# Performance work log

Hardware: AMD Instinct MI355X
Metric: run time of the kernel (lower is better)

## Reference

```python
import jax, jax.numpy as jnp
import numpy as np

N, E, IN, HID, OUT = 40000, 640000, 128, 512, 256


def setup_inputs() -> dict:
    key = jax.random.key(0)
    ks = jax.random.split(key, 8)
    x = jax.random.normal(ks[0], (N, IN), dtype=jnp.float32)
    edge_index = jax.random.randint(ks[1], (2, E), 0, N, dtype=jnp.int64)
    # SAGEConv params: lin_l (applied to aggregated neighbors, with bias),
    # lin_r (applied to root nodes, no bias) -- PyG defaults.
    def lin(k, fin, fout):
        return jax.random.normal(k, (fin, fout), dtype=jnp.float32) / np.sqrt(fin)
    return {
        "x": x,
        "edge_index": edge_index,
        "W1l": lin(ks[2], IN, HID),
        "b1": jnp.zeros((HID,), jnp.float32),
        "W1r": lin(ks[3], IN, HID),
        "W2l": lin(ks[4], HID, OUT),
        "b2": jnp.zeros((OUT,), jnp.float32),
        "W2r": lin(ks[5], HID, OUT),
    }


def _sage_conv(x, src, dst, Wl, b, Wr):
    n = x.shape[0]
    # gather messages from source nodes, mean-aggregate at destination
    msg = x[src]                                            # [E, F]
    agg = jax.ops.segment_sum(msg, dst, num_segments=n)     # [N, F]
    cnt = jax.ops.segment_sum(jnp.ones((src.shape[0],), x.dtype), dst,
                              num_segments=n)               # [N]
    agg = agg / jnp.maximum(cnt, 1.0)[:, None]
    # out = lin_l(mean_neighbors) + lin_r(x)
    return agg @ Wl + b + x @ Wr


def reference(x, edge_index, W1l, b1, W1r, W2l, b2, W2r):
    src, dst = edge_index[0], edge_index[1]
    h = jax.nn.relu(_sage_conv(x, src, dst, W1l, b1, W1r))
    return _sage_conv(h, src, dst, W2l, b2, W2r)
```

## Files before the change

### kernel.cpp

```cpp
#include <hip/hip_runtime.h>


#define N_NODES 40000
#define N_EDGES 640000
#define F_IN 128
#define F_HID 512
#define F_OUT 256
#define NB_SCAN 157

typedef unsigned short ushort_t;
typedef __attribute__((ext_vector_type(8))) short bf16x8;
typedef __attribute__((ext_vector_type(4))) float floatx4;

__device__ __forceinline__ ushort_t f2bf(float f) {
  union { float f; unsigned int u; } x; x.f = f;
  unsigned int r = (x.u + 0x7FFFu + ((x.u >> 16) & 1u)) >> 16;
  return (ushort_t)r;
}
__device__ __forceinline__ float bf2f(ushort_t u) {
  union { unsigned int u; float f; } x; x.u = ((unsigned int)u) << 16;
  return x.f;
}

__global__ void scanA_kernel(const int* __restrict__ deg, int* __restrict__ bsum) {
  __shared__ int sdata[256];
  int i = blockIdx.x * 256 + threadIdx.x;
  sdata[threadIdx.x] = (i < N_NODES) ? deg[i] : 0;
  __syncthreads();
  #pragma unroll
  for (int off = 128; off > 0; off >>= 1) {
    if (threadIdx.x < off) sdata[threadIdx.x] += sdata[threadIdx.x + off];
    __syncthreads();
  }
  if (threadIdx.x == 0) bsum[blockIdx.x] = sdata[0];
}

__global__ void scanB_kernel(const int* __restrict__ bsum, int* __restrict__ boff) {
  __shared__ int buf[2][256];
  int tid = threadIdx.x;
  int v = (tid < NB_SCAN) ? bsum[tid] : 0;
  buf[0][tid] = v;
  __syncthreads();
  int cur = 0;
  #pragma unroll
  for (int off = 1; off < 256; off <<= 1) {
    int val = buf[cur][tid];
    if (tid >= off) val += buf[cur][tid - off];
    buf[cur ^ 1][tid] = val;
    __syncthreads();
    cur ^= 1;
  }
  if (tid < NB_SCAN) boff[tid] = buf[cur][tid] - v;
}

__global__ void scanC_kernel(const int* __restrict__ deg, const int* __restrict__ boff,
                             int* __restrict__ rowptr, int* __restrict__ cursor) {
  __shared__ int buf[2][256];
  int tid = threadIdx.x;
  int i = blockIdx.x * 256 + tid;
  int v = (i < N_NODES) ? deg[i] : 0;
  buf[0][tid] = v;
  __syncthreads();
  int cur = 0;
  #pragma unroll
  for (int off = 1; off < 256; off <<= 1) {
    int val = buf[cur][tid];
    if (tid >= off) val += buf[cur][tid - off];
    buf[cur ^ 1][tid] = val;
    __syncthreads();
    cur ^= 1;
  }
  if (i < N_NODES) {
    int ex = boff[blockIdx.x] + buf[cur][tid] - v;
    rowptr[i] = ex;
    cursor[i] = ex;
    if (i == N_NODES - 1) rowptr[N_NODES] = ex + v;
  }
}

__global__ void fill_kernel(const int* __restrict__ ei, int* __restrict__ cursor,
                            int* __restrict__ col) {
  int e = blockIdx.x * blockDim.x + threadIdx.x;
  if (e < N_EDGES) {
    int d = ei[N_EDGES + e];
    int s = ei[e];
    int pos = atomicAdd(&cursor[d], 1);
    col[pos] = s;
  }
}

__device__ __forceinline__ void wp_body(const float* __restrict__ W,
                                        ushort_t* __restrict__ Wp,
                                        int i, int K, int N, int rowoff, int koff,
                                        int KT) {
  if (i < K * N) {
    int n = i / K, k = i - n * K;
    int ng = rowoff + n, kg = koff + k;
    int gg = ng >> 6, ni = (ng >> 4) & 3, lm = ng & 15;
    int c = kg >> 3, j = kg & 7, t = c >> 2, qk = c & 3;
    size_t dst = (((size_t)(gg * (KT / 32) + t) * 4 + ni) * 64 + qk * 16 + lm) * 8 + j;
    Wp[dst] = f2bf(W[(size_t)k * N + n]);
  }
}

#define PREP_BLOCKS 9038
__global__ void prep_kernel(const float* __restrict__ x, ushort_t* __restrict__ xb,
                            const float* __restrict__ W1l, const float* __restrict__ W1r,
                            const float* __restrict__ W2l, const float* __restrict__ W2r,
                            ushort_t* __restrict__ Wp1, ushort_t* __restrict__ Wp2,
                            const float* __restrict__ b2, float* __restrict__ bc,
                            const int* __restrict__ ei, int* __restrict__ deg) {
  int b = blockIdx.x, tid = threadIdx.x;
  if (b < 5000) {
    int i = b * 256 + tid;
    const int n4 = (N_NODES * F_IN) / 4;
    if (i < n4) {
      float4 v = ((const float4*)x)[i];
      ushort4 o;
      o.x = f2bf(v.x); o.y = f2bf(v.y); o.z = f2bf(v.z); o.w = f2bf(v.w);
      ((ushort4*)xb)[i] = o;
    }
  } else if (b < 5256) {
    wp_body(W1l, Wp1, (b - 5000) * 256 + tid, 128, 512, 0, 0, 256);
  } else if (b < 5512) {
    wp_body(W1r, Wp1, (b - 5256) * 256 + tid, 128, 512, 0, 128, 256);
  } else if (b < 6024) {
    wp_body(W2l, Wp2, (b - 5512) * 256 + tid, 512, 256, 0, 0, 512);
  } else if (b < 6536) {
    wp_body(W2r, Wp2, (b - 6024) * 256 + tid, 512, 256, 256, 0, 512);
  } else if (b < 6538) {
    int i = (b - 6536) * 256 + tid;
    if (i < 512) bc[i] = (i < 256) ? 0.f : b2[i - 256];
  } else {
    int e = (b - 6538) * 256 + tid;
    if (e < N_EDGES) atomicAdd(&deg[ei[N_EDGES + e]], 1);
  }
}

__global__ __launch_bounds__(256) void agg1_kernel(
    const ushort_t* __restrict__ Xb, ushort_t* __restrict__ Yb,
    const int* __restrict__ rowptr, const int* __restrict__ colidx) {
  const int wave = threadIdx.x >> 6, lane = threadIdx.x & 63;
  const int n = blockIdx.x * 4 + wave;
  const int s = rowptr[n], e = rowptr[n + 1];
  float s0 = 0.f, s1 = 0.f;
  for (int base = s; base < e; base += 64) {
    int cnt = min(64, e - base);
    int c = (base + lane < e) ? colidx[base + lane] : 0;
    int j = 0;
    for (; j + 8 <= cnt; j += 8) {
      unsigned int v[8];
      #pragma unroll
      for (int u = 0; u < 8; ++u) {
        int col = __builtin_amdgcn_readlane(c, j + u);
        v[u] = *(const unsigned int*)(Xb + (size_t)col * F_IN + 2 * lane);
      }
      #pragma unroll
      for (int u = 0; u < 8; ++u) {
        s0 += bf2f((ushort_t)(v[u] & 0xffffu));
        s1 += bf2f((ushort_t)(v[u] >> 16));
      }
    }
    for (; j < cnt; ++j) {
      int col = __builtin_amdgcn_readlane(c, j);
      unsigned int v = *(const unsigned int*)(Xb + (size_t)col * F_IN + 2 * lane);
      s0 += bf2f((ushort_t)(v & 0xffffu));
      s1 += bf2f((ushort_t)(v >> 16));
    }
  }
  float inv = 1.f / fmaxf((float)(e - s), 1.f);
  unsigned int o = (unsigned int)f2bf(s0 * inv) | ((unsigned int)f2bf(s1 * inv) << 16);
  *(unsigned int*)(Yb + (size_t)n * F_IN + 2 * lane) = o;
}

__global__ void agg2_kernel(const ushort_t* __restrict__ hl, const float* __restrict__ hr,
                            float* __restrict__ out,
                            const int* __restrict__ rowptr, const int* __restrict__ colidx) {
  __shared__ int cols[128];
  int n = blockIdx.x, f = threadIdx.x;
  int s = rowptr[n], e = rowptr[n + 1];
  float2 hrv = *(const float2*)(hr + (size_t)n * F_OUT + 2 * f);
  float s0 = 0.f, s1 = 0.f;
  for (int base = s; base < e; base += 128) {
    int cnt = min(128, e - base);
    __syncthreads();
    if (f < cnt) cols[f] = colidx[base + f];
    __syncthreads();
    int j = 0;
    for (; j + 8 <= cnt; j += 8) {
      unsigned int v[8];
      #pragma unroll
      for (int u = 0; u < 8; ++u)
        v[u] = *(const unsigned int*)(hl + (size_t)cols[j + u] * F_OUT + 2 * f);
      #pragma unroll
      for (int u = 0; u < 8; ++u) {
        s0 += bf2f((ushort_t)(v[u] & 0xffffu));
        s1 += bf2f((ushort_t)(v[u] >> 16));
      }
    }
    for (; j < cnt; ++j) {
      unsigned int v = *(const unsigned int*)(hl + (size_t)cols[j] * F_OUT + 2 * f);
      s0 += bf2f((ushort_t)(v & 0xffffu));
      s1 += bf2f((ushort_t)(v >> 16));
    }
  }
  float inv = 1.f / fmaxf((float)(e - s), 1.f);
  float2 o;
  o.x = s0 * inv + hrv.x;
  o.y = s1 * inv + hrv.y;
  *(float2*)(out + (size_t)n * F_OUT + 2 * f) = o;
}

__device__ __forceinline__ void mm64(const ushort_t* Pan, int k, int qk, int lm,
                                     bf16x8 f0, bf16x8 f1, bf16x8 f2, bf16x8 f3,
                                     floatx4 (&acc)[4][4]) {
  const int kc = k / 8 + qk;
  #pragma unroll
  for (int mi = 0; mi < 4; ++mi) {
    size_t o = ((size_t)(kc * 64 + mi * 16 + lm) * 16) ^ (size_t)((kc & 7) << 4);
    bf16x8 av = *(const bf16x8*)((const char*)Pan + o);
    acc[mi][0] = __builtin_amdgcn_mfma_f32_16x16x32_bf16(f0, av, acc[mi][0], 0, 0, 0);
    acc[mi][1] = __builtin_amdgcn_mfma_f32_16x16x32_bf16(f1, av, acc[mi][1], 0, 0, 0);
    acc[mi][2] = __builtin_amdgcn_mfma_f32_16x16x32_bf16(f2, av, acc[mi][2], 0, 0, 0);
    acc[mi][3] = __builtin_amdgcn_mfma_f32_16x16x32_bf16(f3, av, acc[mi][3], 0, 0, 0);
  }
}

__global__ __launch_bounds__(512) void gemm_fused(
    const ushort_t* __restrict__ A0,
    const ushort_t* __restrict__ A1,
    const ushort_t* __restrict__ Wp1,
    const float* __restrict__ b1,
    const ushort_t* __restrict__ Wp2,
    const float* __restrict__ bc,
    float* __restrict__ hr, ushort_t* __restrict__ hl) {
  __shared__ ushort_t Pan[64 * 512];
  const int tid = threadIdx.x;
  const int wave = tid >> 6, lane = tid & 63;
  const int lm = lane & 15, qk = lane >> 4;
  const int bm = blockIdx.x * 64;

  const ushort_t* wpg1 = Wp1 + (size_t)wave * 8 * 2048;
  const ushort_t* wpg2 = Wp2 + (size_t)wave * 16 * 2048;
#define LDB1(t, ni) (*(const bf16x8*)(wpg1 + ((size_t)(t) * 4 + (ni)) * 512 + lane * 8))
#define LDB2(t, ni) (*(const bf16x8*)(wpg2 + ((size_t)(t) * 4 + (ni)) * 512 + lane * 8))

  #pragma unroll
  for (int q = 0; q < 4; ++q) {
    int c = tid + q * 512;
    int lc = c & 31;
    int row = c >> 5;
    const ushort_t* src = (lc >= 16)
        ? A1 + (size_t)(bm + row) * 128 + (lc - 16) * 8
        : A0 + (size_t)(bm + row) * 128 + lc * 8;
    bf16x8 v = *(const bf16x8*)src;
    size_t off = ((size_t)(lc * 64 + row) * 16) ^ (size_t)((lc & 7) << 4);
    *(bf16x8*)((char*)Pan + off) = v;
  }

  bf16x8 bvA[4], bvB[4];
  #pragma unroll
  for (int ni = 0; ni < 4; ++ni) bvA[ni] = LDB1(0, ni);
  __syncthreads();

  floatx4 acc1[4][4] = {};
  #pragma unroll 1
  for (int kb = 0; kb < 256; kb += 64) {
    const int t0 = kb / 32;
    #pragma unroll
    for (int ni = 0; ni < 4; ++ni) bvB[ni] = LDB1(t0 + 1, ni);
    mm64(Pan, kb, qk, lm, bvA[0], bvA[1], bvA[2], bvA[3], acc1);
    if (kb + 64 < 256) {
      #pragma unroll
      for (int ni = 0; ni < 4; ++ni) bvA[ni] = LDB1(t0 + 2, ni);
    }
    mm64(Pan, kb + 32, qk, lm, bvB[0], bvB[1], bvB[2], bvB[3], acc1);
  }

  #pragma unroll
  for (int ni = 0; ni < 4; ++ni) bvA[ni] = LDB2(0, ni);
  __syncthreads();

  #pragma unroll
  for (int ni = 0; ni < 4; ++ni) {
    int colg = wave * 64 + ni * 16 + qk * 4;
    float4 b4 = *(const float4*)&b1[colg];
    int lc2 = colg >> 3;
    int sub = (qk & 1) * 8;
    #pragma unroll
    for (int mi = 0; mi < 4; ++mi) {
      int row = mi * 16 + lm;
      ushort4 o;
      o.x = f2bf(fmaxf(acc1[mi][ni][0] + b4.x, 0.f));
      o.y = f2bf(fmaxf(acc1[mi][ni][1] + b4.y, 0.f));
      o.z = f2bf(fmaxf(acc1[mi][ni][2] + b4.z, 0.f));
      o.w = f2bf(fmaxf(acc1[mi][ni][3] + b4.w, 0.f));
      size_t off = (((size_t)(lc2 * 64 + row) * 16) ^ (size_t)((lc2 & 7) << 4)) + sub;
      *(ushort4*)((char*)Pan + off) = o;
    }
  }
  __syncthreads();

  floatx4 acc2[4][4] = {};
  #pragma unroll 1
  for (int kb = 0; kb < 512; kb += 64) {
    const int t0 = kb / 32;
    #pragma unroll
    for (int ni = 0; ni < 4; ++ni) bvB[ni] = LDB2(t0 + 1, ni);
    mm64(Pan, kb, qk, lm, bvA[0], bvA[1], bvA[2], bvA[3], acc2);
    if (kb + 64 < 512) {
      #pragma unroll
      for (int ni = 0; ni < 4; ++ni) bvA[ni] = LDB2(t0 + 2, ni);
    }
    mm64(Pan, kb + 32, qk, lm, bvB[0], bvB[1], bvB[2], bvB[3], acc2);
  }
#undef LDB1
#undef LDB2

  #pragma unroll
  for (int ni = 0; ni < 4; ++ni) {
    int colg = wave * 64 + ni * 16 + qk * 4;
    float4 b4 = *(const float4*)&bc[colg];
    #pragma unroll
    for (int mi = 0; mi < 4; ++mi) {
      int rowg = bm + mi * 16 + lm;
      float v0 = acc2[mi][ni][0] + b4.x;
      float v1 = acc2[mi][ni][1] + b4.y;
      float v2 = acc2[mi][ni][2] + b4.z;
      float v3 = acc2[mi][ni][3] + b4.w;
      if (colg < 256) {
        ushort4 o = {f2bf(v0), f2bf(v1), f2bf(v2), f2bf(v3)};
        *(ushort4*)&hl[(size_t)rowg * 256 + colg] = o;
      } else {
        float4 o = {v0, v1, v2, v3};
        *(float4*)&hr[(size_t)rowg * 256 + (colg - 256)] = o;
      }
    }
  }
}

extern "C" void kernel_launch(void* const* d_in, const int* in_sizes, int n_in,
                              void* d_out, int out_size, void* d_ws, size_t ws_size,
                              hipStream_t stream) {
  const float* x = (const float*)d_in[0];
  const int* ei = (const int*)d_in[1];
  const float* W1l = (const float*)d_in[2];
  const float* b1 = (const float*)d_in[3];
  const float* W1r = (const float*)d_in[4];
  const float* W2l = (const float*)d_in[5];
  const float* b2 = (const float*)d_in[6];
  const float* W2r = (const float*)d_in[7];
  float* out = (float*)d_out;

  char* ws = (char*)d_ws;
  size_t off = 0;
  auto alloc = [&](size_t bytes) {
    void* p = ws + off;
    off = (off + bytes + 255) & ~(size_t)255;
    return p;
  };
  int* deg = (int*)alloc((size_t)N_NODES * 4);
  int* rowptr = (int*)alloc((size_t)(N_NODES + 1) * 4);
  int* cursor = (int*)alloc((size_t)N_NODES * 4);
  int* col = (int*)alloc((size_t)N_EDGES * 4);
  int* bsum = (int*)alloc((size_t)NB_SCAN * 4);
  int* boff = (int*)alloc((size_t)NB_SCAN * 4);
  ushort_t* x_bf = (ushort_t*)alloc((size_t)N_NODES * F_IN * 2);
  ushort_t* aggx_bf = (ushort_t*)alloc((size_t)N_NODES * F_IN * 2);
  ushort_t* hl_bf = (ushort_t*)alloc((size_t)N_NODES * F_OUT * 2);
  float* hr = (float*)alloc((size_t)N_NODES * F_OUT * 4);
  ushort_t* Wp1 = (ushort_t*)alloc((size_t)512 * 256 * 2);
  ushort_t* Wp2 = (ushort_t*)alloc((size_t)512 * 512 * 2);
  float* biascat = (float*)alloc(512 * 4);

  hipMemsetAsync(deg, 0, (size_t)N_NODES * 4, stream);
  prep_kernel<<<PREP_BLOCKS, 256, 0, stream>>>(
      x, x_bf, W1l, W1r, W2l, W2r, Wp1, Wp2, b2, biascat, ei, deg);

  scanA_kernel<<<NB_SCAN, 256, 0, stream>>>(deg, bsum);
  scanB_kernel<<<1, 256, 0, stream>>>(bsum, boff);
  scanC_kernel<<<NB_SCAN, 256, 0, stream>>>(deg, boff, rowptr, cursor);
  fill_kernel<<<(N_EDGES + 255) / 256, 256, 0, stream>>>(ei, cursor, col);

  agg1_kernel<<<N_NODES / 4, 256, 0, stream>>>(x_bf, aggx_bf, rowptr, col);
  gemm_fused<<<625, 512, 0, stream>>>(
      aggx_bf, x_bf, Wp1, b1, Wp2, biascat, hr, hl_bf);
  agg2_kernel<<<N_NODES, 128, 0, stream>>>(hl_bf, hr, out, rowptr, col);
}
```

Before: 274.5 us.

## Fuse layer-1 neighbor mean aggregation into the fused GEMM kernel's LDS panel load

Removes the separate agg1 kernel and its aggx_bf intermediate buffer. Each wave of gemm_fused now gathers and mean-aggregates neighbor features for 8 rows and writes the bf16 result straight into the swizzled LDS panel, while the root x columns are still loaded directly. This drops one kernel launch and a global write plus read of the aggregated features. In exchange, the gather latency now sits inside the GEMM blocks: only 625 blocks of 512 threads with a large LDS panel, so there is less parallelism to hide the irregular memory access.

```diff
diff --git a/kernel.cpp b/kernel.cpp
--- a/kernel.cpp
+++ b/kernel.cpp
@@ -137,42 +137,6 @@
   }
 }
 
-__global__ __launch_bounds__(256) void agg1_kernel(
-    const ushort_t* __restrict__ Xb, ushort_t* __restrict__ Yb,
-    const int* __restrict__ rowptr, const int* __restrict__ colidx) {
-  const int wave = threadIdx.x >> 6, lane = threadIdx.x & 63;
-  const int n = blockIdx.x * 4 + wave;
-  const int s = rowptr[n], e = rowptr[n + 1];
-  float s0 = 0.f, s1 = 0.f;
-  for (int base = s; base < e; base += 64) {
-    int cnt = min(64, e - base);
-    int c = (base + lane < e) ? colidx[base + lane] : 0;
-    int j = 0;
-    for (; j + 8 <= cnt; j += 8) {
-      unsigned int v[8];
-      #pragma unroll
-      for (int u = 0; u < 8; ++u) {
-        int col = __builtin_amdgcn_readlane(c, j + u);
-        v[u] = *(const unsigned int*)(Xb + (size_t)col * F_IN + 2 * lane);
-      }
-      #pragma unroll
-      for (int u = 0; u < 8; ++u) {
-        s0 += bf2f((ushort_t)(v[u] & 0xffffu));
-        s1 += bf2f((ushort_t)(v[u] >> 16));
-      }
-    }
-    for (; j < cnt; ++j) {
-      int col = __builtin_amdgcn_readlane(c, j);
-      unsigned int v = *(const unsigned int*)(Xb + (size_t)col * F_IN + 2 * lane);
-      s0 += bf2f((ushort_t)(v & 0xffffu));
-      s1 += bf2f((ushort_t)(v >> 16));
-    }
-  }
-  float inv = 1.f / fmaxf((float)(e - s), 1.f);
-  unsigned int o = (unsigned int)f2bf(s0 * inv) | ((unsigned int)f2bf(s1 * inv) << 16);
-  *(unsigned int*)(Yb + (size_t)n * F_IN + 2 * lane) = o;
-}
-
 __global__ void agg2_kernel(const ushort_t* __restrict__ hl, const float* __restrict__ hr,
                             float* __restrict__ out,
                             const int* __restrict__ rowptr, const int* __restrict__ colidx) {
@@ -227,8 +191,9 @@
 }
 
 __global__ __launch_bounds__(512) void gemm_fused(
-    const ushort_t* __restrict__ A0,
-    const ushort_t* __restrict__ A1,
+    const ushort_t* __restrict__ Xb,
+    const int* __restrict__ rowptr,
+    const int* __restrict__ colidx,
     const ushort_t* __restrict__ Wp1,
     const float* __restrict__ b1,
     const ushort_t* __restrict__ Wp2,
@@ -245,14 +210,52 @@
 #define LDB1(t, ni) (*(const bf16x8*)(wpg1 + ((size_t)(t) * 4 + (ni)) * 512 + lane * 8))
 #define LDB2(t, ni) (*(const bf16x8*)(wpg2 + ((size_t)(t) * 4 + (ni)) * 512 + lane * 8))
 
-  #pragma unroll
-  for (int q = 0; q < 4; ++q) {
-    int c = tid + q * 512;
-    int lc = c & 31;
-    int row = c >> 5;
-    const ushort_t* src = (lc >= 16)
-        ? A1 + (size_t)(bm + row) * 128 + (lc - 16) * 8
-        : A0 + (size_t)(bm + row) * 128 + lc * 8;
+  #pragma unroll 1
+  for (int i = 0; i < 8; ++i) {
+    int r = wave * 8 + i;
+    int n = bm + r;
+    int s = rowptr[n], e = rowptr[n + 1];
+    float s0 = 0.f, s1 = 0.f;
+    for (int base = s; base < e; base += 64) {
+      int cnt = min(64, e - base);
+      int c = (base + lane < e) ? colidx[base + lane] : 0;
+      int j = 0;
+      for (; j + 8 <= cnt; j += 8) {
+        unsigned int v[8];
+        #pragma unroll
+        for (int u = 0; u < 8; ++u) {
+          int col = __builtin_amdgcn_readlane(c, j + u);
+          v[u] = *(const unsigned int*)(Xb + (size_t)col * F_IN + 2 * lane);
+        }
+        #pragma unroll
+        for (int u = 0; u < 8; ++u) {
+          s0 += bf2f((ushort_t)(v[u] & 0xffffu));
+          s1 += bf2f((ushort_t)(v[u] >> 16));
+        }
+      }
+      for (; j < cnt; ++j) {
+        int col = __builtin_amdgcn_readlane(c, j);
+        unsigned int v = *(const unsigned int*)(Xb + (size_t)col * F_IN + 2 * lane);
+        s0 += bf2f((ushort_t)(v & 0xffffu));
+        s1 += bf2f((ushort_t)(v >> 16));
+      }
+    }
+    float inv = 1.f / fmaxf((float)(e - s), 1.f);
+    unsigned int o = (unsigned int)f2bf(s0 * inv) |
+                     ((unsigned int)f2bf(s1 * inv) << 16);
+    int lc = lane >> 2;
+    size_t off = (((size_t)(lc * 64 + r) * 16) ^ (size_t)((lc & 7) << 4)) +
+                 (size_t)(lane & 3) * 4;
+    *(unsigned int*)((char*)Pan + off) = o;
+  }
+
+  #pragma unroll
+  for (int q = 0; q < 2; ++q) {
+    int cidx = tid + q * 512;
+    int lc16 = cidx & 15;
+    int row = cidx >> 4;
+    int lc = 16 + lc16;
+    const ushort_t* src = Xb + (size_t)(bm + row) * 128 + lc16 * 8;
     bf16x8 v = *(const bf16x8*)src;
     size_t off = ((size_t)(lc * 64 + row) * 16) ^ (size_t)((lc & 7) << 4);
     *(bf16x8*)((char*)Pan + off) = v;
@@ -366,7 +369,6 @@
   int* bsum = (int*)alloc((size_t)NB_SCAN * 4);
   int* boff = (int*)alloc((size_t)NB_SCAN * 4);
   ushort_t* x_bf = (ushort_t*)alloc((size_t)N_NODES * F_IN * 2);
-  ushort_t* aggx_bf = (ushort_t*)alloc((size_t)N_NODES * F_IN * 2);
   ushort_t* hl_bf = (ushort_t*)alloc((size_t)N_NODES * F_OUT * 2);
   float* hr = (float*)alloc((size_t)N_NODES * F_OUT * 4);
   ushort_t* Wp1 = (ushort_t*)alloc((size_t)512 * 256 * 2);
@@ -382,8 +384,7 @@
   scanC_kernel<<<NB_SCAN, 256, 0, stream>>>(deg, boff, rowptr, cursor);
   fill_kernel<<<(N_EDGES + 255) / 256, 256, 0, stream>>>(ei, cursor, col);
 
-  agg1_kernel<<<N_NODES / 4, 256, 0, stream>>>(x_bf, aggx_bf, rowptr, col);
   gemm_fused<<<625, 512, 0, stream>>>(
-      aggx_bf, x_bf, Wp1, b1, Wp2, biascat, hr, hl_bf);
+      x_bf, rowptr, col, Wp1, b1, Wp2, biascat, hr, hl_bf);
   agg2_kernel<<<N_NODES, 128, 0, stream>>>(hl_bf, hr, out, rowptr, col);
 }
```

Measured after the change: 291.2 us. 6.1% more time.

## Fuse CSR scan, fill and first aggregation into one persistent kernel with grid barriers

Applied to the files above, without the earlier changes.

Replaces the three scan kernels, the fill kernel and the first-layer aggregation kernel with a single persistent kernel of 1024 blocks that separates phases with a software grid barrier built on global atomics. The goal is to remove four kernel launches and their inter-kernel gaps. In exchange it depends on all 1024 blocks being co-resident, which is unguaranteed and deadlocks otherwise. It also adds spin-wait barrier overhead, and the aggregation phase now uses grid-stride loops over fewer blocks.

```diff
diff --git a/kernel.cpp b/kernel.cpp
--- a/kernel.cpp
+++ b/kernel.cpp
@@ -7,6 +7,7 @@
 #define F_HID 512
 #define F_OUT 256
 #define NB_SCAN 157
+#define G_CSR 1024
 
 typedef unsigned short ushort_t;
 typedef __attribute__((ext_vector_type(8))) short bf16x8;
@@ -22,71 +23,22 @@
   return x.f;
 }
 
-__global__ void scanA_kernel(const int* __restrict__ deg, int* __restrict__ bsum) {
-  __shared__ int sdata[256];
-  int i = blockIdx.x * 256 + threadIdx.x;
-  sdata[threadIdx.x] = (i < N_NODES) ? deg[i] : 0;
+__device__ __forceinline__ void grid_bar(int* cnt, int* gen) {
   __syncthreads();
-  #pragma unroll
-  for (int off = 128; off > 0; off >>= 1) {
-    if (threadIdx.x < off) sdata[threadIdx.x] += sdata[threadIdx.x + off];
-    __syncthreads();
-  }
-  if (threadIdx.x == 0) bsum[blockIdx.x] = sdata[0];
-}
-
-__global__ void scanB_kernel(const int* __restrict__ bsum, int* __restrict__ boff) {
-  __shared__ int buf[2][256];
-  int tid = threadIdx.x;
-  int v = (tid < NB_SCAN) ? bsum[tid] : 0;
-  buf[0][tid] = v;
+  if (threadIdx.x == 0) {
+    __threadfence();
+    int g = atomicAdd(gen, 0);
+    int v = atomicAdd(cnt, 1);
+    if (v == G_CSR - 1) {
+      atomicExch(cnt, 0);
+      __threadfence();
+      atomicAdd(gen, 1);
+    } else {
+      while (atomicAdd(gen, 0) == g) __builtin_amdgcn_s_sleep(2);
+    }
+    __threadfence();
+  }
   __syncthreads();
-  int cur = 0;
-  #pragma unroll
-  for (int off = 1; off < 256; off <<= 1) {
-    int val = buf[cur][tid];
-    if (tid >= off) val += buf[cur][tid - off];
-    buf[cur ^ 1][tid] = val;
-    __syncthreads();
-    cur ^= 1;
-  }
-  if (tid < NB_SCAN) boff[tid] = buf[cur][tid] - v;
-}
-
-__global__ void scanC_kernel(const int* __restrict__ deg, const int* __restrict__ boff,
-                             int* __restrict__ rowptr, int* __restrict__ cursor) {
-  __shared__ int buf[2][256];
-  int tid = threadIdx.x;
-  int i = blockIdx.x * 256 + tid;
-  int v = (i < N_NODES) ? deg[i] : 0;
-  buf[0][tid] = v;
-  __syncthreads();
-  int cur = 0;
-  #pragma unroll
-  for (int off = 1; off < 256; off <<= 1) {
-    int val = buf[cur][tid];
-    if (tid >= off) val += buf[cur][tid - off];
-    buf[cur ^ 1][tid] = val;
-    __syncthreads();
-    cur ^= 1;
-  }
-  if (i < N_NODES) {
-    int ex = boff[blockIdx.x] + buf[cur][tid] - v;
-    rowptr[i] = ex;
-    cursor[i] = ex;
-    if (i == N_NODES - 1) rowptr[N_NODES] = ex + v;
-  }
-}
-
-__global__ void fill_kernel(const int* __restrict__ ei, int* __restrict__ cursor,
-                            int* __restrict__ col) {
-  int e = blockIdx.x * blockDim.x + threadIdx.x;
-  if (e < N_EDGES) {
-    int d = ei[N_EDGES + e];
-    int s = ei[e];
-    int pos = atomicAdd(&cursor[d], 1);
-    col[pos] = s;
-  }
 }
 
 __device__ __forceinline__ void wp_body(const float* __restrict__ W,
@@ -137,40 +89,112 @@
   }
 }
 
-__global__ __launch_bounds__(256) void agg1_kernel(
+__global__ __launch_bounds__(256, 4) void csr_agg1_kernel(
+    const int* __restrict__ deg, int* __restrict__ bsum, int* __restrict__ boff,
+    int* __restrict__ rowptr, int* __restrict__ cursor,
+    const int* __restrict__ ei, int* __restrict__ col,
     const ushort_t* __restrict__ Xb, ushort_t* __restrict__ Yb,
-    const int* __restrict__ rowptr, const int* __restrict__ colidx) {
-  const int wave = threadIdx.x >> 6, lane = threadIdx.x & 63;
-  const int n = blockIdx.x * 4 + wave;
-  const int s = rowptr[n], e = rowptr[n + 1];
-  float s0 = 0.f, s1 = 0.f;
-  for (int base = s; base < e; base += 64) {
-    int cnt = min(64, e - base);
-    int c = (base + lane < e) ? colidx[base + lane] : 0;
-    int j = 0;
-    for (; j + 8 <= cnt; j += 8) {
-      unsigned int v[8];
-      #pragma unroll
-      for (int u = 0; u < 8; ++u) {
-        int col = __builtin_amdgcn_readlane(c, j + u);
-        v[u] = *(const unsigned int*)(Xb + (size_t)col * F_IN + 2 * lane);
+    int* bar_cnt, int* bar_gen) {
+  const int bid = blockIdx.x, tid = threadIdx.x;
+  __shared__ int sdata[256];
+  __shared__ int buf[2][256];
+
+  for (int t = bid; t < NB_SCAN; t += G_CSR) {
+    int i = t * 256 + tid;
+    sdata[tid] = (i < N_NODES) ? deg[i] : 0;
+    __syncthreads();
+    #pragma unroll
+    for (int off = 128; off > 0; off >>= 1) {
+      if (tid < off) sdata[tid] += sdata[tid + off];
+      __syncthreads();
+    }
+    if (tid == 0) bsum[t] = sdata[0];
+    __syncthreads();
+  }
+  grid_bar(bar_cnt, bar_gen);
+
+  if (bid == 0) {
+    int v = (tid < NB_SCAN) ? bsum[tid] : 0;
+    buf[0][tid] = v;
+    __syncthreads();
+    int cur = 0;
+    #pragma unroll
+    for (int off = 1; off < 256; off <<= 1) {
+      int val = buf[cur][tid];
+      if (tid >= off) val += buf[cur][tid - off];
+      buf[cur ^ 1][tid] = val;
+      __syncthreads();
+      cur ^= 1;
+    }
+    if (tid < NB_SCAN) boff[tid] = buf[cur][tid] - v;
+  }
+  grid_bar(bar_cnt, bar_gen);
+
+  for (int t = bid; t < NB_SCAN; t += G_CSR) {
+    int i = t * 256 + tid;
+    int v = (i < N_NODES) ? deg[i] : 0;
+    buf[0][tid] = v;
+    __syncthreads();
+    int cur = 0;
+    #pragma unroll
+    for (int off = 1; off < 256; off <<= 1) {
+      int val = buf[cur][tid];
+      if (tid >= off) val += buf[cur][tid - off];
+      buf[cur ^ 1][tid] = val;
+      __syncthreads();
+      cur ^= 1;
+    }
+    if (i < N_NODES) {
+      int ex = boff[t] + buf[cur][tid] - v;
+      rowptr[i] = ex;
+      cursor[i] = ex;
+      if (i == N_NODES - 1) rowptr[N_NODES] = ex + v;
+    }
+    __syncthreads();
+  }
+  grid_bar(bar_cnt, bar_gen);
+
+  for (int e = bid * 256 + tid; e < N_EDGES; e += G_CSR * 256) {
+    int d = ei[N_EDGES + e];
+    int s = ei[e];
+    int pos = atomicAdd(&cursor[d], 1);
+    col[pos] = s;
+  }
+  grid_bar(bar_cnt, bar_gen);
+
+  const int wave = tid >> 6, lane = tid & 63;
+  for (int n = bid * 4 + wave; n < N_NODES; n += G_CSR * 4) {
+    const int s = rowptr[n], e = rowptr[n + 1];
+    float s0 = 0.f, s1 = 0.f;
+    for (int base = s; base < e; base += 64) {
+      int cnt = min(64, e - base);
+      int c = (base + lane < e) ? col[base + lane] : 0;
+      int j = 0;
+      for (; j + 8 <= cnt; j += 8) {
+        unsigned int v[8];
+        #pragma unroll
+        for (int u = 0; u < 8; ++u) {
+          int cc = __builtin_amdgcn_readlane(c, j + u);
+          v[u] = *(const unsigned int*)(Xb + (size_t)cc * F_IN + 2 * lane);
+        }
+        #pragma unroll
+        for (int u = 0; u < 8; ++u) {
+          s0 += bf2f((ushort_t)(v[u] & 0xffffu));
+          s1 += bf2f((ushort_t)(v[u] >> 16));
+        }
       }
-      #pragma unroll
-      for (int u = 0; u < 8; ++u) {
-        s0 += bf2f((ushort_t)(v[u] & 0xffffu));
-        s1 += bf2f((ushort_t)(v[u] >> 16));
+      for (; j < cnt; ++j) {
+        int cc = __builtin_amdgcn_readlane(c, j);
+        unsigned int v = *(const unsigned int*)(Xb + (size_t)cc * F_IN + 2 * lane);
+        s0 += bf2f((ushort_t)(v & 0xffffu));
+        s1 += bf2f((ushort_t)(v >> 16));
       }
     }
-    for (; j < cnt; ++j) {
-      int col = __builtin_amdgcn_readlane(c, j);
-      unsigned int v = *(const unsigned int*)(Xb + (size_t)col * F_IN + 2 * lane);
-      s0 += bf2f((ushort_t)(v & 0xffffu));
-      s1 += bf2f((ushort_t)(v >> 16));
-    }
-  }
-  float inv = 1.f / fmaxf((float)(e - s), 1.f);
-  unsigned int o = (unsigned int)f2bf(s0 * inv) | ((unsigned int)f2bf(s1 * inv) << 16);
-  *(unsigned int*)(Yb + (size_t)n * F_IN + 2 * lane) = o;
+    float inv = 1.f / fmaxf((float)(e - s), 1.f);
+    unsigned int o = (unsigned int)f2bf(s0 * inv) |
+                     ((unsigned int)f2bf(s1 * inv) << 16);
+    *(unsigned int*)(Yb + (size_t)n * F_IN + 2 * lane) = o;
+  }
 }
 
 __global__ void agg2_kernel(const ushort_t* __restrict__ hl, const float* __restrict__ hr,
@@ -359,7 +383,9 @@
     off = (off + bytes + 255) & ~(size_t)255;
     return p;
   };
-  int* deg = (int*)alloc((size_t)N_NODES * 4);
+  int* deg = (int*)alloc((size_t)(N_NODES + 64) * 4);
+  int* bar_cnt = deg + N_NODES;
+  int* bar_gen = deg + N_NODES + 1;
   int* rowptr = (int*)alloc((size_t)(N_NODES + 1) * 4);
   int* cursor = (int*)alloc((size_t)N_NODES * 4);
   int* col = (int*)alloc((size_t)N_EDGES * 4);
@@ -373,16 +399,15 @@
   ushort_t* Wp2 = (ushort_t*)alloc((size_t)512 * 512 * 2);
   float* biascat = (float*)alloc(512 * 4);
 
-  hipMemsetAsync(deg, 0, (size_t)N_NODES * 4, stream);
+  hipMemsetAsync(deg, 0, (size_t)(N_NODES + 64) * 4, stream);
+
   prep_kernel<<<PREP_BLOCKS, 256, 0, stream>>>(
       x, x_bf, W1l, W1r, W2l, W2r, Wp1, Wp2, b2, biascat, ei, deg);
 
-  scanA_kernel<<<NB_SCAN, 256, 0, stream>>>(deg, bsum);
-  scanB_kernel<<<1, 256, 0, stream>>>(bsum, boff);
-  scanC_kernel<<<NB_SCAN, 256, 0, stream>>>(deg, boff, rowptr, cursor);
-  fill_kernel<<<(N_EDGES + 255) / 256, 256, 0, stream>>>(ei, cursor, col);
-
-  agg1_kernel<<<N_NODES / 4, 256, 0, stream>>>(x_bf, aggx_bf, rowptr, col);
+  csr_agg1_kernel<<<G_CSR, 256, 0, stream>>>(
+      deg, bsum, boff, rowptr, cursor, ei, col, x_bf, aggx_bf,
+      bar_cnt, bar_gen);
+
   gemm_fused<<<625, 512, 0, stream>>>(
       aggx_bf, x_bf, Wp1, b1, Wp2, biascat, hr, hl_bf);
   agg2_kernel<<<N_NODES, 128, 0, stream>>>(hl_bf, hr, out, rowptr, col);
```

Measured after the change: 596.4 us. 2.17x slower.
